# Kernel tuning notes

Hardware: AMD Instinct MI355X
Metric: run time of the kernel (lower is better)

The kernel has to match this reference:

```python
import jax, jax.numpy as jnp
import numpy as np
from jax import lax

B = 8192
HS = 64        # hidden_size (output channels)
HS4 = HS + 4   # internal channel count (68)
K = 3          # conv kernel size


def setup_inputs() -> dict:
    key = jax.random.key(0)
    ks = jax.random.split(key, 16)
    def n(k, shape, s=1.0):
        return jax.random.normal(k, shape, dtype=jnp.float32) * s
    return {
        "x": n(ks[0], (B, HS, 6, 6)),
        "cell": n(ks[1], (B, 2)),
        "interspace_coord": n(ks[2], (B, 2, 6, 6)),
        "conv1_w": n(ks[3], (HS4, HS4, K, K), 0.05),
        "conv1_b": n(ks[4], (HS4,), 0.05),
        "conv3_w": n(ks[5], (HS4, HS4, K, K), 0.05),
        "conv3_b": n(ks[6], (HS4,), 0.05),
        "lin5_w": n(ks[7], (9 * HS, HS4 * 25), 0.02),
        "lin5_b": n(ks[8], (9 * HS,), 0.02),
        "lin4_w": n(ks[9], (9 * HS, HS4 * 16), 0.02),
        "lin4_b": n(ks[10], (9 * HS,), 0.02),
        "lin3_w": n(ks[11], (9 * HS, HS4 * 9), 0.02),
        "lin3_b": n(ks[12], (9 * HS,), 0.02),
        "final_w": n(ks[13], (HS, 9 * HS), 0.02),
        "final_b": n(ks[14], (HS,), 0.02),
    }


def _conv(z, w, b):
    # torch Conv2d with padding=k//2, stride 1 == SAME conv, NCHW/OIHW
    y = lax.conv_general_dilated(z, w, (1, 1), 'SAME',
                                 dimension_numbers=('NCHW', 'OIHW', 'NCHW'))
    return y + b[None, :, None, None]


def _corners(z, ws):
    # four corner windows, stacked on a new leading axis (corner-major)
    H, W = z.shape[-2:]
    return jnp.stack([z[..., :ws, :ws],
                      z[..., :ws, W - ws:],
                      z[..., H - ws:, :ws],
                      z[..., H - ws:, W - ws:]], axis=0)


def reference(x, cell, interspace_coord,
              conv1_w, conv1_b, conv3_w, conv3_b,
              lin5_w, lin5_b, lin4_w, lin4_b, lin3_w, lin3_b,
              final_w, final_b):
    Bn = x.shape[0]
    new_cell = jnp.broadcast_to(cell.reshape(Bn, -1)[:, :, None, None],
                                (Bn, 2, 6, 6))
    lins = {5: (lin5_w, lin5_b), 4: (lin4_w, lin4_b), 3: (lin3_w, lin3_b)}
    for ws in (5, 4, 3):
        z = jnp.concatenate([x, new_cell, interspace_coord], axis=1)  # [B,68,6,6]
        z = _corners(z, ws).reshape(-1, HS4, ws, ws)                  # [4B,68,ws,ws]
        z = jnp.sin(z) + jnp.cos(z)
        z = jax.nn.relu(_conv(z, conv1_w, conv1_b))
        z = jnp.sin(z) + jnp.cos(z)
        z = jax.nn.relu(_conv(z, conv3_w, conv3_b)).reshape(4, Bn, -1)
        Wl, bl = lins[ws]
        z = jax.nn.relu(z @ Wl.T + bl).reshape(4, Bn, HS, 3, 3)
        m = jnp.concatenate([z[0], z[1]], axis=-1)   # [B,64,3,6]
        n = jnp.concatenate([z[2], z[3]], axis=-1)
        x = jnp.concatenate([m, n], axis=-2)          # [B,64,6,6]
    ew = 3
    c = _corners(x, ew)                               # [4,B,64,3,3]
    c = c.reshape(4 * Bn, -1) @ final_w.T + final_b   # [4B,64]
    c = c.reshape(Bn, HS, 2, 2)                       # same flat-order reshape as torch
    xc = x[:, :, ew - 1:ew + 1, ew - 1:ew + 1]        # center 2x2
    return (xc * c).reshape(Bn, HS, -1)
```

## Files before the change

kernel.cpp:

```cpp
#include <hip/hip_runtime.h>
#include <hip/hip_bf16.h>
#include <cstdint>
#include <cstddef>

#define BN 8192
#define MTOT 32768

using bf16 = __hip_bfloat16;
typedef float f32x4 __attribute__((ext_vector_type(4)));
typedef short short8 __attribute__((ext_vector_type(8)));

__device__ __forceinline__ bf16 f2b(float v) { return __float2bfloat16(v); }
__device__ __forceinline__ float b2f(bf16 v) { return __bfloat162float(v); }
__device__ __forceinline__ float sincos_sum(float x) {
    return 1.41421356237f * __sinf(x + 0.78539816340f);
}


__global__ __launch_bounds__(256)
void zprep_block(const float* __restrict__ xF, const float* __restrict__ cell,
                 const float* __restrict__ isc, bf16* __restrict__ Z,
                 int m0g, int CM)
{
    constexpr int KD = 1728, KTRUE = 1700;
    const int b = blockIdx.x, tid = threadIdx.x;
    __shared__ float s[68][37];

    for (int i = tid; i < 64 * 36; i += 256) {
        int ic = i / 36, off = i % 36;
        s[ic][off] = sincos_sum(xF[((size_t)b * 64 + ic) * 36 + off]);
    }
    if (tid < 2) {
        float t = sincos_sum(cell[b * 2 + tid]);
        #pragma unroll
        for (int off = 0; off < 36; off++) s[64 + tid][off] = t;
    }
    if (tid >= 64 && tid < 136) {
        int j = tid - 64;
        int ic = j / 36, off = j % 36;
        s[66 + ic][off] = sincos_sum(isc[((size_t)b * 2 + ic) * 36 + off]);
    }
    __syncthreads();

    for (int i = tid; i < 4 * KD; i += 256) {
        int q = i / KD, k = i % KD;
        int gm = q * BN + b;
        if (gm < m0g || gm >= m0g + CM) continue;
        float v = 0.f;
        if (k < KTRUE) {
            int pi = k / 68, ic = k % 68;
            int r = (q >> 1) + pi / 5;
            int c = (q & 1) + pi % 5;
            v = s[ic][r * 6 + c];
        }
        Z[(size_t)(gm - m0g) * KD + k] = f2b(v);
    }
}

template<int WSv>
__device__ __forceinline__ bf16 conv_elem(const float* __restrict__ src, int n, int k)
{
    constexpr int KTRUE = 68 * WSv * WSv;
    float v = 0.f;
    if (n < KTRUE && k < KTRUE) {
        int po = n / 68, oc = n % 68, ro = po / WSv, co = po % WSv;
        int pi = k / 68, ic = k % 68, ri = pi / WSv, ci = pi % WSv;
        int kr = ri - ro + 1, kc = ci - co + 1;
        if (kr >= 0 && kr < 3 && kc >= 0 && kc < 3)
            v = src[((oc * 68 + ic) * 3 + kr) * 3 + kc];
    }
    return f2b(v);
}
template<int WSv>
__device__ __forceinline__ bf16 lin_elem(const float* __restrict__ wl, int n, int k)
{
    constexpr int KTRUE = 68 * WSv * WSv;
    float v = 0.f;
    if (n < 576 && k < KTRUE) {
        int pi = k / 68, ic = k % 68;
        v = wl[(size_t)n * KTRUE + ic * (WSv * WSv) + pi];
    }
    return f2b(v);
}

__global__ void megabuild(const float* __restrict__ c1w, const float* __restrict__ c3w,
                          const float* __restrict__ l5w, const float* __restrict__ l4w,
                          const float* __restrict__ l3w, const float* __restrict__ fw,
                          const float* __restrict__ c1b, const float* __restrict__ c3b,
                          const float* __restrict__ bl5, const float* __restrict__ bl4,
                          const float* __restrict__ bl3, const float* __restrict__ bfin,
                          const float* __restrict__ cell, const float* __restrict__ isc,
                          bf16* __restrict__ w1d5, bf16* __restrict__ w3d5,
                          bf16* __restrict__ w1d4, bf16* __restrict__ w3d4,
                          bf16* __restrict__ w1d3, bf16* __restrict__ w3d3,
                          bf16* __restrict__ wl5p, bf16* __restrict__ wl4p,
                          bf16* __restrict__ wl3p, bf16* __restrict__ wfp,
                          float* __restrict__ bias,
                          bf16* __restrict__ Z4, bf16* __restrict__ Z3)
{
    constexpr unsigned S0 = 2u*1792*1728, S1 = 2u*1152*1088, S2 = 2u*640*640;
    constexpr unsigned S3 = 640u*1728, S4 = 640u*1088, S5 = 640u*640;
    constexpr unsigned S6 = 128u*576, S7 = 9216;
    constexpr unsigned S8 = 4u*8192*16*4, S9 = 4u*8192*9*4, S10 = 32768u*28;
    constexpr unsigned O1=S0, O2=O1+S1, O3=O2+S2, O4=O3+S3, O5=O4+S4, O6=O5+S5,
                       O7=O6+S6, O8=O7+S7, O9=O8+S8, O10=O9+S9, OT=O10+S10;
    unsigned e = blockIdx.x * 256u + threadIdx.x;
    if (e >= OT) return;
    if (e < O1) {
        constexpr unsigned per = 1792u*1728;
        unsigned i = (e < per) ? e : e - per;
        bf16* dst = (e < per) ? w1d5 : w3d5;
        const float* src = (e < per) ? c1w : c3w;
        dst[i] = conv_elem<5>(src, (int)(i / 1728u), (int)(i % 1728u));
    } else if (e < O2) {
        unsigned i0 = e - O1; constexpr unsigned per = 1152u*1088;
        unsigned i = (i0 < per) ? i0 : i0 - per;
        bf16* dst = (i0 < per) ? w1d4 : w3d4;
        const float* src = (i0 < per) ? c1w : c3w;
        dst[i] = conv_elem<4>(src, (int)(i / 1088u), (int)(i % 1088u));
    } else if (e < O3) {
        unsigned i0 = e - O2; constexpr unsigned per = 640u*640;
        unsigned i = (i0 < per) ? i0 : i0 - per;
        bf16* dst = (i0 < per) ? w1d3 : w3d3;
        const float* src = (i0 < per) ? c1w : c3w;
        dst[i] = conv_elem<3>(src, (int)(i / 640u), (int)(i % 640u));
    } else if (e < O4) {
        unsigned i = e - O3;
        wl5p[i] = lin_elem<5>(l5w, (int)(i / 1728u), (int)(i % 1728u));
    } else if (e < O5) {
        unsigned i = e - O4;
        wl4p[i] = lin_elem<4>(l4w, (int)(i / 1088u), (int)(i % 1088u));
    } else if (e < O6) {
        unsigned i = e - O5;
        wl3p[i] = lin_elem<3>(l3w, (int)(i / 640u), (int)(i % 640u));
    } else if (e < O7) {
        unsigned i = e - O6, n = i / 576u, k = i % 576u;
        wfp[i] = (n < 64u) ? f2b(fw[n * 576u + k]) : f2b(0.f);
    } else if (e < O8) {
        int i = (int)(e - O7);
        float v = 0.f;
        if (i < 1792)      { int n = i;        if (n < 1700) v = c1b[n % 68]; }
        else if (i < 3584) { int n = i - 1792; if (n < 1700) v = c3b[n % 68]; }
        else if (i < 4736) { int n = i - 3584; if (n < 1088) v = c1b[n % 68]; }
        else if (i < 5888) { int n = i - 4736; if (n < 1088) v = c3b[n % 68]; }
        else if (i < 6528) { int n = i - 5888; if (n < 612)  v = c1b[n % 68]; }
        else if (i < 7168) { int n = i - 6528; if (n < 612)  v = c3b[n % 68]; }
        else if (i < 7808) { int n = i - 7168; if (n < 576)  v = bl5[n]; }
        else if (i < 8448) { int n = i - 7808; if (n < 576)  v = bl4[n]; }
        else if (i < 9088) { int n = i - 8448; if (n < 576)  v = bl3[n]; }
        else               { int n = i - 9088; if (n < 64)   v = bfin[n]; }
        bias[i] = v;
    } else if (e < O9) {
        unsigned i = e - O8;
        int j = (int)(i & 3u); i >>= 2;
        int pi = (int)(i & 15u); i >>= 4;
        int b = (int)(i & 8191u); int q = (int)(i >> 13);
        float t;
        if (j < 2) t = cell[b * 2 + j];
        else {
            int r = (q >> 1) * 2 + pi / 4, c = (q & 1) * 2 + pi % 4;
            t = isc[((size_t)b * 2 + (j - 2)) * 36 + r * 6 + c];
        }
        Z4[((size_t)q * BN + b) * 1088 + pi * 68 + 64 + j] = f2b(sincos_sum(t));
    } else if (e < O10) {
        unsigned i = e - O9;
        int j = (int)(i & 3u); i >>= 2;
        int pi = (int)(i % 9u); i /= 9u;
        int b = (int)(i & 8191u); int q = (int)(i >> 13);
        float t;
        if (j < 2) t = cell[b * 2 + j];
        else {
            int r = (q >> 1) * 3 + pi / 3, c = (q & 1) * 3 + pi % 3;
            t = isc[((size_t)b * 2 + (j - 2)) * 36 + r * 6 + c];
        }
        Z3[((size_t)q * BN + b) * 640 + pi * 68 + 64 + j] = f2b(sincos_sum(t));
    } else {
        unsigned i = e - O10;
        int m = (int)(i / 28u), t = (int)(i % 28u);
        Z3[(size_t)m * 640 + 612 + t] = f2b(0.f);
    }
}

__device__ __forceinline__ void gload_lds16(const bf16* g, const bf16* lds_wave_base)
{
    unsigned off = (unsigned)(uintptr_t)lds_wave_base;
    off = __builtin_amdgcn_readfirstlane(off);
    __builtin_amdgcn_global_load_lds((const __attribute__((address_space(1))) unsigned int*)g,
                                     (__attribute__((address_space(3))) unsigned int*)off,
                                     16, 0, 0);
}

__device__ __forceinline__ int imin(int a, int b) { return a < b ? a : b; }
__device__ __forceinline__ int imax(int a, int b) { return a > b ? a : b; }

template<int EPI, int WS, int WN>
__global__ __launch_bounds__(512, 2)
void gemm8(const bf16* __restrict__ A, const bf16* __restrict__ Bm, int KD,
           const float* __restrict__ bias, int ntiles,
           bf16* __restrict__ C, int ldc, int nlimit,
           int m0g, bf16* __restrict__ znext)
{
    __shared__ bf16 As[3][16384];
    __shared__ bf16 Bs[3][4096];
    const int tid = threadIdx.x;
    const int wave = tid >> 6, lane = tid & 63;
    const int l15 = lane & 15, lq = lane >> 4;
    const int wr = wave * 64;

    const int id = blockIdx.x;
    const int mt8 = (int)gridDim.x / (ntiles * 8);
    const int xcd = id & 7, local = id >> 3;
    const int m_idx = xcd * mt8 + local / ntiles;
    const int n_idx = local % ntiles;
    const int n0 = n_idx * 128, m0 = m_idx * 512;

    int s0b = 0, s0e = KD, s1b = 0, s1e = 0, s2b = 0, s2e = 0;
    if (WS > 0) {
        int po_lo = imin(n0 / 68, WS * WS - 1);
        int po_hi = imin((n0 + 127) / 68, WS * WS - 1);
        int ro_lo = po_lo / WS, ro_hi = po_hi / WS;
        int r_lo = imax(ro_lo - 1, 0), r_hi = imin(ro_hi + 1, WS - 1);
        int ci_lo = 0, ci_hi = WS - 1;
        if (ro_lo == ro_hi) {
            ci_lo = imax(po_lo % WS - 1, 0);
            ci_hi = imin(po_hi % WS + 1, WS - 1);
        }
        if (ci_lo == 0 && ci_hi == WS - 1) {
            s0b = (r_lo * WS * 68) & ~31;
            s0e = imin(KD, ((r_hi + 1) * WS * 68 + 31) & ~31);
        } else {
            s0b = ((r_lo * WS + ci_lo) * 68) & ~31;
            s0e = imin(KD, (((r_lo * WS + ci_hi + 1) * 68) + 31) & ~31);
            if (r_hi > r_lo) {
                s1b = (((r_lo + 1) * WS + ci_lo) * 68) & ~31;
                s1e = imin(KD, ((((r_lo + 1) * WS + ci_hi + 1) * 68) + 31) & ~31);
            }
            if (r_hi > r_lo + 1) {
                s2b = (((r_lo + 2) * WS + ci_lo) * 68) & ~31;
                s2e = imin(KD, ((((r_lo + 2) * WS + ci_hi + 1) * 68) + 31) & ~31);
            }
        }
    }
    const int c0 = (s0e - s0b) >> 5;
    const int c1 = c0 + ((s1e - s1b) >> 5);
    const int nt = c1 + ((s2e - s2b) >> 5);
    auto k0_of = [&](int t2) -> int {
        int k = s0b + (t2 << 5);
        if (t2 >= c0) k = s1b + ((t2 - c0) << 5);
        if (t2 >= c1) k = s2b + ((t2 - c1) << 5);
        return k;
    };

    const int srow = tid >> 2;
    const int sc8 = (tid & 3) ^ (srow & 3);
    const bf16* aSrc = A + (size_t)(m0 + srow) * KD + sc8 * 8;
    const bf16* bSrc = Bm + (size_t)(n0 + srow) * KD + sc8 * 8;
    const int sOff = srow * 32 + (tid & 3) * 8;

    auto stageA01 = [&](int k0, int buf) {
        gload_lds16(aSrc + k0, &As[buf][sOff]);
        gload_lds16(aSrc + k0 + (size_t)128 * KD, &As[buf][sOff + 4096]);
    };
    auto stageA23 = [&](int k0, int buf) {
        gload_lds16(aSrc + k0 + (size_t)256 * KD, &As[buf][sOff + 8192]);
        gload_lds16(aSrc + k0 + (size_t)384 * KD, &As[buf][sOff + 12288]);
    };
    auto stageB = [&](int k0, int buf) {
        gload_lds16(bSrc + k0, &Bs[buf][sOff]);
    };

    const int lrA = wr + l15;
    const int offA0 = lrA * 32 + ((lq ^ (lrA & 3)) * 8);
    const int offB0 = l15 * 32 + ((lq ^ (l15 & 3)) * 8);

    f32x4 acc[4][8];
    #pragma unroll
    for (int i = 0; i < 4; i++)
        #pragma unroll
        for (int j = 0; j < 8; j++) { f32x4 z = {0.f, 0.f, 0.f, 0.f}; acc[i][j] = z; }

    {
        const int k0a = k0_of(0);
        stageA01(k0a, 0); stageA23(k0a, 0); stageB(k0a, 0);
        if (nt > 1) {
            const int k0b = k0_of(1);
            stageA01(k0b, 1); stageA23(k0b, 1); stageB(k0b, 1);
        }
        __syncthreads();
    }

    for (int t = 0; t < nt; ++t) {
        const int cur = t % 3;
        const int nx = (t + 2) % 3;
        const bool pf = (t + 2) < nt;
        int k2 = 0;
        if (pf) k2 = k0_of(t + 2);

        const bf16* Ac = &As[cur][0];
        const bf16* Bc = &Bs[cur][0];

        short8 af[4], bg[4];
        #pragma unroll
        for (int i = 0; i < 4; i++) af[i] = *(const short8*)&Ac[offA0 + i * 512];
        #pragma unroll
        for (int j = 0; j < 4; j++) bg[j] = *(const short8*)&Bc[offB0 + j * 512];
        if (pf) stageA01(k2, nx);
        __builtin_amdgcn_s_barrier();
        asm volatile("s_waitcnt lgkmcnt(0)" ::: "memory");
        __builtin_amdgcn_sched_barrier(0);
        __builtin_amdgcn_s_setprio(1);
        #pragma unroll
        for (int i = 0; i < 4; i++)
            #pragma unroll
            for (int j = 0; j < 4; j++)
                acc[i][j] = __builtin_amdgcn_mfma_f32_16x16x32_bf16(af[i], bg[j], acc[i][j], 0, 0, 0);
        __builtin_amdgcn_s_setprio(0);
        __builtin_amdgcn_s_barrier();

        short8 bh[4];
        #pragma unroll
        for (int j = 0; j < 4; j++) bh[j] = *(const short8*)&Bc[offB0 + (j + 4) * 512];
        if (pf) {
            stageA23(k2, nx); stageB(k2, nx);
            asm volatile("s_waitcnt vmcnt(5)" ::: "memory");
        } else {
            asm volatile("s_waitcnt vmcnt(0)" ::: "memory");
        }
        __builtin_amdgcn_s_barrier();
        asm volatile("s_waitcnt lgkmcnt(0)" ::: "memory");
        __builtin_amdgcn_sched_barrier(0);
        __builtin_amdgcn_s_setprio(1);
        #pragma unroll
        for (int i = 0; i < 4; i++)
            #pragma unroll
            for (int j = 0; j < 4; j++)
                acc[i][j + 4] = __builtin_amdgcn_mfma_f32_16x16x32_bf16(af[i], bh[j], acc[i][j + 4], 0, 0, 0);
        __builtin_amdgcn_s_setprio(0);
        __builtin_amdgcn_s_barrier();
    }

    float bj[8];
    #pragma unroll
    for (int j = 0; j < 8; j++) bj[j] = bias[n0 + j * 16 + l15];

    #pragma unroll
    for (int i = 0; i < 4; i++) {
        #pragma unroll
        for (int j = 0; j < 8; j++) {
            int n = n0 + j * 16 + l15;
            #pragma unroll
            for (int r = 0; r < 4; r++) {
                int m = m0 + wr + i * 16 + lq * 4 + r;
                float v = acc[i][j][r];
                if (EPI == 0) {
                    if (n < nlimit) {
                        v += bj[j]; v = fmaxf(v, 0.f); v = sincos_sum(v);
                        C[(size_t)m * ldc + n] = f2b(v);
                    }
                } else if (EPI == 1) {
                    if (n < nlimit) {
                        v += bj[j]; v = fmaxf(v, 0.f);
                        C[(size_t)m * ldc + n] = f2b(v);
                    }
                } else {
                    if (n < 576) {
                        v += bj[j]; v = fmaxf(v, 0.f);
                        bf16 tv = f2b(sincos_sum(v));
                        int gm = m0g + m;
                        int q = gm >> 13, b = gm & (BN - 1);
                        int ch = n / 9, p = n % 9;
                        int R = p / 3 + (q >> 1) * 3, Cc = p % 3 + (q & 1) * 3;
                        constexpr int OFF = 6 - WN;
                        constexpr int KDN = (WN == 4) ? 1088 : 640;
                        #pragma unroll
                        for (int qr = 0; qr < 2; qr++) {
                            int rr = R - OFF * qr;
                            if (rr < 0 || rr >= WN) continue;
                            #pragma unroll
                            for (int qc = 0; qc < 2; qc++) {
                                int cc = Cc - OFF * qc;
                                if (cc < 0 || cc >= WN) continue;
                                int pi = rr * WN + cc;
                                znext[((size_t)((qr * 2 + qc) * BN + b)) * KDN + pi * 68 + ch] = tv;
                            }
                        }
                    }
                }
            }
        }
    }
}

template<int EPI, int WS, int WN>
__global__ __launch_bounds__(256)
void gemm_bt(const bf16* __restrict__ A, const bf16* __restrict__ Bm, int KD,
             const float* __restrict__ bias, int ntiles,
             bf16* __restrict__ C, int ldc, int nlimit,
             int m0g, bf16* __restrict__ znext,
             const bf16* __restrict__ afin_xc, float* __restrict__ outp)
{
    __shared__ bf16 As[128 * 32];
    __shared__ bf16 Bs[128 * 32];
    const int tid = threadIdx.x;
    const int wave = tid >> 6, lane = tid & 63;
    const int l15 = lane & 15, lq = lane >> 4;
    const int wr = (wave >> 1) * 64, wc = (wave & 1) * 64;

    const int id = blockIdx.x;
    const int mt8 = (int)gridDim.x / (ntiles * 8);
    const int xcd = id & 7, local = id >> 3;
    const int m_idx = xcd * mt8 + local / ntiles;
    const int n_idx = local % ntiles;
    const int n0 = n_idx * 128, m0 = m_idx * 128;

    int nspans = 1, sbeg[4], send[4];
    sbeg[0] = 0; send[0] = KD;
    if (WS > 0) {
        int po_lo = imin(n0 / 68, WS * WS - 1);
        int po_hi = imin((n0 + 127) / 68, WS * WS - 1);
        int ro_lo = po_lo / WS, ro_hi = po_hi / WS;
        int r_lo = imax(ro_lo - 1, 0), r_hi = imin(ro_hi + 1, WS - 1);
        int ci_lo = 0, ci_hi = WS - 1;
        if (ro_lo == ro_hi) {
            ci_lo = imax(po_lo % WS - 1, 0);
            ci_hi = imin(po_hi % WS + 1, WS - 1);
        }
        if (ci_lo == 0 && ci_hi == WS - 1) {
            sbeg[0] = (r_lo * WS * 68) & ~31;
            send[0] = imin(KD, ((r_hi + 1) * WS * 68 + 31) & ~31);
        } else {
            nspans = 0;
            for (int ri = r_lo; ri <= r_hi; ri++) {
                sbeg[nspans] = ((ri * WS + ci_lo) * 68) & ~31;
                send[nspans] = imin(KD, (((ri * WS + ci_hi + 1) * 68) + 31) & ~31);
                nspans++;
            }
        }
    }

    float bj[4];
    #pragma unroll
    for (int j = 0; j < 4; j++) bj[j] = bias[n0 + wc + j * 16 + l15];

    const bf16* Ab = A + (size_t)m0 * KD;
    const bf16* Bb = Bm + (size_t)n0 * KD;
    const int srow = tid >> 2, scol = (tid & 3) * 8;
    const bf16* aG0 = Ab + (size_t)srow * KD + scol;
    const bf16* aG1 = Ab + (size_t)(srow + 64) * KD + scol;
    const bf16* bG0 = Bb + (size_t)srow * KD + scol;
    const bf16* bG1 = Bb + (size_t)(srow + 64) * KD + scol;
    const bf16* lA0 = &As[wave * 512];
    const bf16* lA1 = &As[2048 + wave * 512];
    const bf16* lB0 = &Bs[wave * 512];
    const bf16* lB1 = &Bs[2048 + wave * 512];

    f32x4 acc[4][4];
    #pragma unroll
    for (int i = 0; i < 4; i++)
        #pragma unroll
        for (int j = 0; j < 4; j++) { f32x4 z = {0.f, 0.f, 0.f, 0.f}; acc[i][j] = z; }

    for (int s = 0; s < nspans; s++) {
        for (int k0 = sbeg[s]; k0 < send[s]; k0 += 32) {
            gload_lds16(aG0 + k0, lA0);
            gload_lds16(aG1 + k0, lA1);
            gload_lds16(bG0 + k0, lB0);
            gload_lds16(bG1 + k0, lB1);
            __syncthreads();
            short8 af[4], bg[4];
            #pragma unroll
            for (int i = 0; i < 4; i++) af[i] = *(const short8*)&As[(wr + i * 16 + l15) * 32 + lq * 8];
            #pragma unroll
            for (int j = 0; j < 4; j++) bg[j] = *(const short8*)&Bs[(wc + j * 16 + l15) * 32 + lq * 8];
            #pragma unroll
            for (int i = 0; i < 4; i++)
                #pragma unroll
                for (int j = 0; j < 4; j++)
                    acc[i][j] = __builtin_amdgcn_mfma_f32_16x16x32_bf16(af[i], bg[j], acc[i][j], 0, 0, 0);
            __syncthreads();
        }
    }

    #pragma unroll
    for (int i = 0; i < 4; i++) {
        #pragma unroll
        for (int j = 0; j < 4; j++) {
            int n = n0 + wc + j * 16 + l15;
            #pragma unroll
            for (int r = 0; r < 4; r++) {
                int m = m0 + wr + i * 16 + lq * 4 + r;
                float v = acc[i][j][r];
                if (EPI == 0) {
                    if (n < nlimit) {
                        v += bj[j]; v = fmaxf(v, 0.f); v = sincos_sum(v);
                        C[(size_t)m * ldc + n] = f2b(v);
                    }
                } else if (EPI == 1) {
                    if (n < nlimit) {
                        v += bj[j]; v = fmaxf(v, 0.f);
                        C[(size_t)m * ldc + n] = f2b(v);
                    }
                } else if (EPI == 2) {
                    if (n < 576) {
                        v += bj[j]; v = fmaxf(v, 0.f);
                        bf16 t = f2b(sincos_sum(v));
                        int gm = m0g + m;
                        int q = gm >> 13, b = gm & (BN - 1);
                        int ch = n / 9, p = n % 9;
                        int R = p / 3 + (q >> 1) * 3, Cc = p % 3 + (q & 1) * 3;
                        constexpr int OFF = 6 - WN;
                        constexpr int KDN = (WN == 4) ? 1088 : 640;
                        #pragma unroll
                        for (int qr = 0; qr < 2; qr++) {
                            int rr = R - OFF * qr;
                            if (rr < 0 || rr >= WN) continue;
                            #pragma unroll
                            for (int qc = 0; qc < 2; qc++) {
                                int cc = Cc - OFF * qc;
                                if (cc < 0 || cc >= WN) continue;
                                int pi = rr * WN + cc;
                                znext[((size_t)((qr * 2 + qc) * BN + b)) * KDN + pi * 68 + ch] = t;
                            }
                        }
                    }
                } else {
                    if (n < 64) {
                        v += bj[j];
                        int gm = m0g + m;
                        int f = gm * 64 + n;
                        int b2 = f >> 8, rem = f & 255;
                        int ch2 = rem >> 2, ii = (rem >> 1) & 1, jj = rem & 1;
                        int qq = ii * 2 + jj;
                        const int offt[4] = {8, 6, 2, 0};
                        float xc = b2f(afin_xc[((size_t)qq * BN + b2) * 576 + ch2 * 9 + offt[qq]]);
                        outp[f] = v * xc;
                    }
                }
            }
        }
    }
}

extern "C" void kernel_launch(void* const* d_in, const int* in_sizes, int n_in,
                              void* d_out, int out_size, void* d_ws, size_t ws_size,
                              hipStream_t stream)
{
    const float* x    = (const float*)d_in[0];
    const float* cell = (const float*)d_in[1];
    const float* isc  = (const float*)d_in[2];
    const float* c1w  = (const float*)d_in[3];
    const float* c1b  = (const float*)d_in[4];
    const float* c3w  = (const float*)d_in[5];
    const float* c3b  = (const float*)d_in[6];
    const float* l5w  = (const float*)d_in[7];
    const float* l5b  = (const float*)d_in[8];
    const float* l4w  = (const float*)d_in[9];
    const float* l4b  = (const float*)d_in[10];
    const float* l3w  = (const float*)d_in[11];
    const float* l3b  = (const float*)d_in[12];
    const float* fw   = (const float*)d_in[13];
    const float* fb   = (const float*)d_in[14];

    char* base = (char*)d_ws;
    size_t cur = 0;
    auto take = [&](size_t bytes) -> char* {
        char* r = base + cur; cur += (bytes + 255) & ~(size_t)255; return r;
    };

    const size_t Z4B = (size_t)MTOT * 1088 * 2;
    const size_t Z3B = (size_t)MTOT * 640 * 2;
    const size_t AFB = (size_t)MTOT * 576 * 2;
    size_t wbytes = 2 * (1792ull * 1728 + 1152ull * 1088 + 640ull * 640) * 2
                  + (640ull * 1728 + 640ull * 1088 + 640ull * 640) * 2
                  + 128ull * 576 * 2 + 9216ull * 4 + 64 * 256;
    auto need = [&](int nc) -> size_t {
        return Z4B + Z3B + AFB + wbytes + 2 * ((size_t)(MTOT / nc) * 1728 * 2);
    };
    const bool use8 = (ws_size >= need(8));
    int nchunk = use8 ? ((ws_size >= need(1)) ? 1 : (ws_size >= need(2)) ? 2
                       : (ws_size >= need(4)) ? 4 : 8)
                      : 16;

    bf16* Z4   = (bf16*)take(Z4B);
    bf16* Z3   = (bf16*)take(Z3B);
    bf16* afinb = (bf16*)take(AFB);
    bf16* w1d5 = (bf16*)take(1792ull * 1728 * 2);
    bf16* w3d5 = (bf16*)take(1792ull * 1728 * 2);
    bf16* w1d4 = (bf16*)take(1152ull * 1088 * 2);
    bf16* w3d4 = (bf16*)take(1152ull * 1088 * 2);
    bf16* w1d3 = (bf16*)take(640ull * 640 * 2);
    bf16* w3d3 = (bf16*)take(640ull * 640 * 2);
    bf16* wl5p = (bf16*)take(640ull * 1728 * 2);
    bf16* wl4p = (bf16*)take(640ull * 1088 * 2);
    bf16* wl3p = (bf16*)take(640ull * 640 * 2);
    bf16* wfp  = (bf16*)take(128ull * 576 * 2);
    float* biasb = (float*)take(9216ull * 4);
    int CM = MTOT / nchunk;
    int mt = CM / 128;
    int mt5 = CM / 512;
    bf16* Za = (bf16*)take((size_t)CM * 1728 * 2);
    bf16* Zb = (bf16*)take((size_t)CM * 1728 * 2);

    {
        constexpr unsigned OT = 2u*1792*1728 + 2u*1152*1088 + 2u*640*640
                              + 640u*1728 + 640u*1088 + 640u*640 + 128u*576 + 9216
                              + 4u*8192*16*4 + 4u*8192*9*4 + 32768u*28;
        megabuild<<<(OT + 255) / 256, 256, 0, stream>>>(
            c1w, c3w, l5w, l4w, l3w, fw, c1b, c3b, l5b, l4b, l3b, fb, cell, isc,
            w1d5, w3d5, w1d4, w3d4, w1d3, w3d3, wl5p, wl4p, wl3p, wfp, biasb, Z4, Z3);
    }

    if (use8) {
        for (int c = 0; c < nchunk; c++) {
            int m0g = c * CM;
            zprep_block<<<BN, 256, 0, stream>>>(x, cell, isc, Za, m0g, CM);
            gemm8<0, 5, 0><<<14 * mt5, 512, 0, stream>>>(Za, w1d5, 1728, biasb + 0, 14,
                                                         Zb, 1728, 1728, 0, nullptr);
            gemm8<1, 5, 0><<<14 * mt5, 512, 0, stream>>>(Zb, w3d5, 1728, biasb + 1792, 14,
                                                         Za, 1728, 1728, 0, nullptr);
            gemm8<2, 0, 4><<<5 * mt5, 512, 0, stream>>>(Za, wl5p, 1728, biasb + 7168, 5,
                                                        nullptr, 0, 0, m0g, Z4);
        }
        for (int c = 0; c < nchunk; c++) {
            int m0g = c * CM;
            gemm8<0, 4, 0><<<9 * mt5, 512, 0, stream>>>(Z4 + (size_t)m0g * 1088, w1d4, 1088,
                                                        biasb + 3584, 9, Zb, 1088, 1088,
                                                        0, nullptr);
            gemm8<1, 4, 0><<<9 * mt5, 512, 0, stream>>>(Zb, w3d4, 1088, biasb + 4736, 9,
                                                        Za, 1088, 1088, 0, nullptr);
            gemm8<2, 0, 3><<<5 * mt5, 512, 0, stream>>>(Za, wl4p, 1088, biasb + 7808, 5,
                                                        nullptr, 0, 0, m0g, Z3);
        }
        for (int c = 0; c < nchunk; c++) {
            int m0g = c * CM;
            gemm8<0, 3, 0><<<5 * mt5, 512, 0, stream>>>(Z3 + (size_t)m0g * 640, w1d3, 640,
                                                        biasb + 5888, 5, Zb, 640, 640,
                                                        0, nullptr);
            gemm8<1, 3, 0><<<5 * mt5, 512, 0, stream>>>(Zb, w3d3, 640, biasb + 6528, 5,
                                                        Za, 640, 640, 0, nullptr);
            gemm8<1, 0, 0><<<5 * mt5, 512, 0, stream>>>(Za, wl3p, 640, biasb + 8448, 5,
                                                        afinb + (size_t)m0g * 576, 576, 576,
                                                        0, nullptr);
        }
    } else {
        for (int c = 0; c < nchunk; c++) {
            int m0g = c * CM;
            zprep_block<<<BN, 256, 0, stream>>>(x, cell, isc, Za, m0g, CM);
            gemm_bt<0, 5, 0><<<14 * mt, 256, 0, stream>>>(Za, w1d5, 1728, biasb + 0, 14,
                                                          Zb, 1728, 1728, 0, nullptr, nullptr, nullptr);
            gemm_bt<1, 5, 0><<<14 * mt, 256, 0, stream>>>(Zb, w3d5, 1728, biasb + 1792, 14,
                                                          Za, 1728, 1728, 0, nullptr, nullptr, nullptr);
            gemm_bt<2, 0, 4><<<5 * mt, 256, 0, stream>>>(Za, wl5p, 1728, biasb + 7168, 5,
                                                         nullptr, 0, 0, m0g, Z4, nullptr, nullptr);
        }
        for (int c = 0; c < nchunk; c++) {
            int m0g = c * CM;
            gemm_bt<0, 4, 0><<<9 * mt, 256, 0, stream>>>(Z4 + (size_t)m0g * 1088, w1d4, 1088,
                                                         biasb + 3584, 9, Zb, 1088, 1088,
                                                         0, nullptr, nullptr, nullptr);
            gemm_bt<1, 4, 0><<<9 * mt, 256, 0, stream>>>(Zb, w3d4, 1088, biasb + 4736, 9,
                                                         Za, 1088, 1088, 0, nullptr, nullptr, nullptr);
            gemm_bt<2, 0, 3><<<5 * mt, 256, 0, stream>>>(Za, wl4p, 1088, biasb + 7808, 5,
                                                         nullptr, 0, 0, m0g, Z3, nullptr, nullptr);
        }
        for (int c = 0; c < nchunk; c++) {
            int m0g = c * CM;
            gemm_bt<0, 3, 0><<<5 * mt, 256, 0, stream>>>(Z3 + (size_t)m0g * 640, w1d3, 640,
                                                         biasb + 5888, 5, Zb, 640, 640,
                                                         0, nullptr, nullptr, nullptr);
            gemm_bt<1, 3, 0><<<5 * mt, 256, 0, stream>>>(Zb, w3d3, 640, biasb + 6528, 5,
                                                         Za, 640, 640, 0, nullptr, nullptr, nullptr);
            gemm_bt<1, 0, 0><<<5 * mt, 256, 0, stream>>>(Za, wl3p, 640, biasb + 8448, 5,
                                                         afinb + (size_t)m0g * 576, 576, 576,
                                                         0, nullptr, nullptr, nullptr);
        }
    }
    for (int c = 0; c < nchunk; c++) {
        int m0g = c * CM;
        gemm_bt<3, 0, 0><<<mt, 256, 0, stream>>>(afinb + (size_t)m0g * 576, wfp, 576,
                                                 biasb + 9088, 1, nullptr, 0, 0, m0g,
                                                 nullptr, afinb, (float*)d_out);
    }
}
```

Before: 1.426 ms.

## Merge two-phase GEMM loop into one barrier per k-step and retune LDS swizzle

The GEMM main loop previously split each k-step into two halves, each with its own barriers and staging. Now all eight B fragments are loaded at once, the whole next-next stage is prefetched in one go, and a single barrier ends each iteration. The LDS XOR swizzle now uses (row>>1)&3 instead of row&3, consistently for global-to-LDS stores and fragment reads, aiming to reduce bank conflicts with 64-byte rows. The aim is fewer barriers and less synchronisation stalling. In exchange, more fragment registers are live at once, and the finer interleaving of loads with MFMA work is lost.

```diff
diff --git a/kernel.cpp b/kernel.cpp
--- a/kernel.cpp
+++ b/kernel.cpp
@@ -252,7 +252,7 @@
     };
 
     const int srow = tid >> 2;
-    const int sc8 = (tid & 3) ^ (srow & 3);
+    const int sc8 = (tid & 3) ^ ((srow >> 1) & 3);
     const bf16* aSrc = A + (size_t)(m0 + srow) * KD + sc8 * 8;
     const bf16* bSrc = Bm + (size_t)(n0 + srow) * KD + sc8 * 8;
     const int sOff = srow * 32 + (tid & 3) * 8;
@@ -270,8 +270,8 @@
     };
 
     const int lrA = wr + l15;
-    const int offA0 = lrA * 32 + ((lq ^ (lrA & 3)) * 8);
-    const int offB0 = l15 * 32 + ((lq ^ (l15 & 3)) * 8);
+    const int offA0 = lrA * 32 + ((lq ^ ((l15 >> 1) & 3)) * 8);
+    const int offB0 = l15 * 32 + ((lq ^ ((l15 >> 1) & 3)) * 8);
 
     f32x4 acc[4][8];
     #pragma unroll
@@ -293,49 +293,31 @@
         const int cur = t % 3;
         const int nx = (t + 2) % 3;
         const bool pf = (t + 2) < nt;
-        int k2 = 0;
-        if (pf) k2 = k0_of(t + 2);
 
         const bf16* Ac = &As[cur][0];
         const bf16* Bc = &Bs[cur][0];
 
-        short8 af[4], bg[4];
+        short8 af[4], bg[8];
         #pragma unroll
         for (int i = 0; i < 4; i++) af[i] = *(const short8*)&Ac[offA0 + i * 512];
         #pragma unroll
-        for (int j = 0; j < 4; j++) bg[j] = *(const short8*)&Bc[offB0 + j * 512];
-        if (pf) stageA01(k2, nx);
-        __builtin_amdgcn_s_barrier();
-        asm volatile("s_waitcnt lgkmcnt(0)" ::: "memory");
-        __builtin_amdgcn_sched_barrier(0);
+        for (int j = 0; j < 8; j++) bg[j] = *(const short8*)&Bc[offB0 + j * 512];
+
+        if (pf) {
+            const int k2 = k0_of(t + 2);
+            stageA01(k2, nx); stageA23(k2, nx); stageB(k2, nx);
+        }
+
         __builtin_amdgcn_s_setprio(1);
         #pragma unroll
         for (int i = 0; i < 4; i++)
             #pragma unroll
-            for (int j = 0; j < 4; j++)
+            for (int j = 0; j < 8; j++)
                 acc[i][j] = __builtin_amdgcn_mfma_f32_16x16x32_bf16(af[i], bg[j], acc[i][j], 0, 0, 0);
         __builtin_amdgcn_s_setprio(0);
-        __builtin_amdgcn_s_barrier();
-
-        short8 bh[4];
-        #pragma unroll
-        for (int j = 0; j < 4; j++) bh[j] = *(const short8*)&Bc[offB0 + (j + 4) * 512];
-        if (pf) {
-            stageA23(k2, nx); stageB(k2, nx);
-            asm volatile("s_waitcnt vmcnt(5)" ::: "memory");
-        } else {
-            asm volatile("s_waitcnt vmcnt(0)" ::: "memory");
-        }
-        __builtin_amdgcn_s_barrier();
-        asm volatile("s_waitcnt lgkmcnt(0)" ::: "memory");
-        __builtin_amdgcn_sched_barrier(0);
-        __builtin_amdgcn_s_setprio(1);
-        #pragma unroll
-        for (int i = 0; i < 4; i++)
-            #pragma unroll
-            for (int j = 0; j < 4; j++)
-                acc[i][j + 4] = __builtin_amdgcn_mfma_f32_16x16x32_bf16(af[i], bh[j], acc[i][j + 4], 0, 0, 0);
-        __builtin_amdgcn_s_setprio(0);
+
+        if (pf) asm volatile("s_waitcnt vmcnt(5)" ::: "memory");
+        else    asm volatile("s_waitcnt vmcnt(0)" ::: "memory");
         __builtin_amdgcn_s_barrier();
     }
 
```

New measurement: 1.322 ms. -7.3%, faster.
